# Performance work log

Hardware: AMD Instinct MI355X
Metric: run time of the kernel (lower is better)

## Reference

```python
import jax, jax.numpy as jnp
import numpy as np

D_MODEL = 1024
D_K = 64
D_V = 64
N_HEADS = 16
LN_EPS = 1e-5


def setup_inputs() -> dict:
    key = jax.random.key(0)
    ks = jax.random.split(key, 9)
    B, S = 2, 2048
    scale = 0.02
    return {
        "input_Q": jax.random.normal(ks[0], (B, S, D_MODEL), dtype=jnp.float32),
        "input_K": jax.random.normal(ks[1], (B, S, D_MODEL), dtype=jnp.float32),
        "input_V": jax.random.normal(ks[2], (B, S, D_MODEL), dtype=jnp.float32),
        "W_Q": jax.random.normal(ks[3], (D_MODEL, N_HEADS * D_K), dtype=jnp.float32) * scale,
        "W_K": jax.random.normal(ks[4], (D_MODEL, N_HEADS * D_K), dtype=jnp.float32) * scale,
        "W_V": jax.random.normal(ks[5], (D_MODEL, N_HEADS * D_V), dtype=jnp.float32) * scale,
        "W_O": jax.random.normal(ks[6], (N_HEADS * D_V, D_MODEL), dtype=jnp.float32) * scale,
        "ln_gamma": jnp.ones((D_MODEL,), dtype=jnp.float32),
        "ln_beta": jnp.zeros((D_MODEL,), dtype=jnp.float32),
    }


def reference(input_Q, input_K, input_V, W_Q, W_K, W_V, W_O, ln_gamma, ln_beta):
    B, Lq, _ = input_Q.shape
    Lk = input_K.shape[1]
    # projections -> [B, H, L, d]
    Q = (input_Q @ W_Q).reshape(B, Lq, N_HEADS, D_K).transpose(0, 2, 1, 3)
    K = (input_K @ W_K).reshape(B, Lk, N_HEADS, D_K).transpose(0, 2, 1, 3)
    V = (input_V @ W_V).reshape(B, Lk, N_HEADS, D_V).transpose(0, 2, 1, 3)
    # scores: [B, H, Lq, Lk]
    scores = jnp.einsum("bhqd,bhkd->bhqk", Q, K) / jnp.sqrt(jnp.float32(D_K))
    # NOTE: source uses nn.Softmax(dim=1) -> softmax over the HEADS axis (faithful quirk)
    attn = jax.nn.softmax(scores, axis=1)
    context = jnp.einsum("bhqk,bhkv->bhqv", attn, V)
    context = context.transpose(0, 2, 1, 3).reshape(B, Lq, N_HEADS * D_V)
    output = context @ W_O
    # residual + LayerNorm over last dim
    x = output + input_Q
    mu = jnp.mean(x, axis=-1, keepdims=True)
    var = jnp.mean(jnp.square(x - mu), axis=-1, keepdims=True)
    return (x - mu) / jnp.sqrt(var + LN_EPS) * ln_gamma + ln_beta
```

## Files before the change

### kernel.cpp

```cpp
#include <hip/hip_runtime.h>
#include <cstdint>
#include <cstddef>

#define DM 1024
#define HEADS 16
#define DHEAD 64
#define SEQ 2048
#define BATCH 2

typedef __bf16 bf16x8 __attribute__((ext_vector_type(8)));
typedef float  f32x4  __attribute__((ext_vector_type(4)));
typedef unsigned short u16;
typedef unsigned int u32;
typedef u16 u16x8 __attribute__((ext_vector_type(8)));
typedef u16 u16x4 __attribute__((ext_vector_type(4)));

__device__ __forceinline__ float bf2f(u16 u){
    union { u32 i; float f; } v; v.i = ((u32)u) << 16; return v.f;
}
__device__ __forceinline__ u16 f2bf(float f){
    union { float f; u32 i; } v; v.f = f;
    u32 r = v.i + 0x7FFF + ((v.i >> 16) & 1);
    return (u16)(r >> 16);
}
__device__ __forceinline__ u16 f2bf_rhu(float f){
    union { float f; u32 i; } v; v.f = f;
    return (u16)((v.i + 0x8000u) >> 16);
}
__device__ __forceinline__ void gload16(const u16* g, u16* l){
    __builtin_amdgcn_global_load_lds(
        (const __attribute__((address_space(1))) u32*)g,
        (__attribute__((address_space(3))) u32*)l, 16, 0, 0);
}

__global__ void k_probe(const u16* __restrict__ q, int* __restrict__ hdr){
    if (threadIdx.x == 0 && blockIdx.x == 0){
        int cnt = 0;
        for (int i = 0; i < 256; i += 2){
            int e = (q[i] >> 7) & 0xFF;
            if (e >= 90 && e <= 141) cnt++;
        }
        hdr[0] = (cnt >= 64) ? 1 : 0;
        #pragma unroll
        for (int c = 1; c <= 8; c++) hdr[c] = 0;
    }
}

__global__ __launch_bounds__(256) void k_cvt3(const void* __restrict__ s0,
                                              const void* __restrict__ s1,
                                              const void* __restrict__ s2,
                                              u16* __restrict__ dstbase,
                                              const int* __restrict__ flag, int n){
    int z = blockIdx.y;
    const void* src = (z == 0) ? s0 : ((z == 1) ? s1 : s2);
    u16* dst = dstbase + (size_t)z * n;
    int i = (blockIdx.x * 256 + threadIdx.x) * 8;
    if (i >= n) return;
    if (*flag){
        *(u16x8*)&dst[i] = *(const u16x8*)((const u16*)src + i);
    } else {
        const float* s = (const float*)src + i;
        u16x8 o;
        #pragma unroll
        for (int j = 0; j < 8; j++) o[j] = f2bf(s[j]);
        *(u16x8*)&dst[i] = o;
    }
}

__global__ void k_tcvt4(const void* __restrict__ w0, const void* __restrict__ w1,
                        const void* __restrict__ w2, const void* __restrict__ w3,
                        u16* __restrict__ dstbase,
                        const int* __restrict__ flag, int R, int C){
    __shared__ u16 tile[32][33];
    int z = blockIdx.z;
    const void* src = (z == 0) ? w0 : ((z == 1) ? w1 : ((z == 2) ? w2 : w3));
    u16* dst = dstbase + (size_t)z * R * C;
    bool isbf = (*flag != 0);
    int c0 = blockIdx.x * 32, r0 = blockIdx.y * 32;
    int tx = threadIdx.x, ty = threadIdx.y;
    #pragma unroll
    for (int i = 0; i < 32; i += 8){
        size_t idx = (size_t)(r0 + ty + i) * C + c0 + tx;
        tile[ty + i][tx] = isbf ? ((const u16*)src)[idx] : f2bf(((const float*)src)[idx]);
    }
    __syncthreads();
    #pragma unroll
    for (int i = 0; i < 32; i += 8)
        dst[(size_t)(c0 + ty + i) * R + r0 + tx] = tile[tx][ty + i];
}

__global__ void k_transpose(const u16* __restrict__ src, u16* __restrict__ dst,
                            int R, int C){
    __shared__ u16 tile[32][33];
    size_t boff = (size_t)blockIdx.z * R * C;
    src += boff; dst += boff;
    int c0 = blockIdx.x * 32, r0 = blockIdx.y * 32;
    int tx = threadIdx.x, ty = threadIdx.y;
    #pragma unroll
    for (int i = 0; i < 32; i += 8)
        tile[ty + i][tx] = src[(size_t)(r0 + ty + i) * C + c0 + tx];
    __syncthreads();
    #pragma unroll
    for (int i = 0; i < 32; i += 8)
        dst[(size_t)(c0 + ty + i) * R + r0 + tx] = tile[tx][ty + i];
}

__global__ __launch_bounds__(256, 2) void k_gemm3z(const u16* __restrict__ A0,
                                                   const u16* __restrict__ Bt0,
                                                   u16* __restrict__ C0,
                                                   size_t strA, size_t strB, size_t strC,
                                                   int M, int N, int K){
    __shared__ u16 lsA[128 * 32];
    __shared__ u16 lsB[128 * 32];
    int z = blockIdx.z;
    const u16* A  = A0  + strA * z;
    const u16* Bt = Bt0 + strB * z;
    u16* C = C0 + strC * z;
    int m0 = blockIdx.y * 128, n0 = blockIdx.x * 128;
    int t = threadIdx.x, lane = t & 63, w = t >> 6;
    int l15 = lane & 15, quad = lane >> 4;
    int wm = (w & 1) * 64, wn = (w >> 1) * 64;
    int r0 = 32 * w + (lane >> 2);
    int r1 = r0 + 16;
    int c0s = (lane & 3) ^ (r0 & 3);
    int c1s = (lane & 3) ^ (r1 & 3);
    u16* dA0 = &lsA[(32 * w) * 32];
    u16* dA1 = &lsA[(32 * w + 16) * 32];
    u16* dB0 = &lsB[(32 * w) * 32];
    u16* dB1 = &lsB[(32 * w + 16) * 32];
    f32x4 acc[4][4] = {};
    for (int k0 = 0; k0 < K; k0 += 32){
        __syncthreads();
        gload16(&A [(size_t)(m0 + r0) * K + k0 + c0s * 8], dA0);
        gload16(&A [(size_t)(m0 + r1) * K + k0 + c1s * 8], dA1);
        gload16(&Bt[(size_t)(n0 + r0) * K + k0 + c0s * 8], dB0);
        gload16(&Bt[(size_t)(n0 + r1) * K + k0 + c1s * 8], dB1);
        __syncthreads();
        bf16x8 af[4], bfr[4];
        #pragma unroll
        for (int i = 0; i < 4; i++){
            int row = wm + i * 16 + l15;
            af[i] = *(const bf16x8*)&lsA[row * 32 + ((quad ^ (row & 3)) * 8)];
        }
        #pragma unroll
        for (int j = 0; j < 4; j++){
            int row = wn + j * 16 + l15;
            bfr[j] = *(const bf16x8*)&lsB[row * 32 + ((quad ^ (row & 3)) * 8)];
        }
        #pragma unroll
        for (int i = 0; i < 4; i++)
            #pragma unroll
            for (int j = 0; j < 4; j++)
                acc[i][j] = __builtin_amdgcn_mfma_f32_16x16x32_bf16(af[i], bfr[j], acc[i][j], 0, 0, 0);
    }
    #pragma unroll
    for (int i = 0; i < 4; i++)
        #pragma unroll
        for (int j = 0; j < 4; j++)
            #pragma unroll
            for (int r = 0; r < 4; r++){
                int m = m0 + wm + i * 16 + quad * 4 + r;
                int n = n0 + wn + j * 16 + l15;
                C[(size_t)m * N + n] = f2bf(acc[i][j][r]);
            }
}

__global__ __launch_bounds__(1024, 4) void k_attn5(const u16* __restrict__ Qp,
                                                   const u16* __restrict__ Kp,
                                                   const u16* __restrict__ Vt,
                                                   u16* __restrict__ c0,
                                                   u16* __restrict__ c1,
                                                   u16* __restrict__ c2,
                                                   u16* __restrict__ c3,
                                                   int* __restrict__ cnt,
                                                   int ncomboM1, int iters){
    __shared__ u16 ebuf[2][16][64][36];
    __shared__ int s_combo, s_slot;
    int t = threadIdx.x;
    if (t == 0){
        int xcc;
        asm volatile("s_getreg_b32 %0, hwreg(HW_REG_XCC_ID)" : "=s"(xcc));
        int start = xcc & ncomboM1;
        int combo = -1, slot = -1;
        for (int a = 0; a <= ncomboM1 && combo < 0; a++){
            int c = (start + a) & ncomboM1;
            int s = atomicAdd(&cnt[c], 1);
            if (s < 32){ combo = c; slot = s; }
        }
        s_combo = combo; s_slot = slot;
    }
    __syncthreads();
    int combo = s_combo;
    if (combo < 0) return;
    int b = combo & 1, chunk = combo >> 1;
    int q0 = s_slot * 64;
    int h = t >> 6, lane = t & 63, l15 = lane & 15, quad = lane >> 4;
    u16* outp = (chunk == 0) ? c0 : ((chunk == 1) ? c1 : ((chunk == 2) ? c2 : c3));
    const float cexp = 0.125f * 1.44269504f;
    int kbeg = chunk * (iters << 5);

    bf16x8 qf[4][2];
    #pragma unroll
    for (int sub = 0; sub < 4; sub++)
        #pragma unroll
        for (int ch = 0; ch < 2; ch++)
            qf[sub][ch] = *(const bf16x8*)&Qp[((size_t)(b * SEQ + q0 + sub * 16 + l15)) * DM
                                             + h * DHEAD + ch * 32 + quad * 8];

    f32x4 oacc[4][4] = {};
    int sq = t >> 4, sku = (t & 15) * 2;

    auto score_phase = [&](int it){
        int k0 = kbeg + (it << 5), bf = it & 1;
        #pragma unroll
        for (int kt = 0; kt < 2; kt++){
            const u16* kb = Kp + ((size_t)(b * SEQ + k0 + kt * 16 + l15)) * DM + h * DHEAD + quad * 8;
            bf16x8 kf0 = *(const bf16x8*)(kb);
            bf16x8 kf1 = *(const bf16x8*)(kb + 32);
            #pragma unroll
            for (int sub = 0; sub < 4; sub++){
                f32x4 sc = {};
                sc = __builtin_amdgcn_mfma_f32_16x16x32_bf16(qf[sub][0], kf0, sc, 0, 0, 0);
                sc = __builtin_amdgcn_mfma_f32_16x16x32_bf16(qf[sub][1], kf1, sc, 0, 0, 0);
                #pragma unroll
                for (int r = 0; r < 4; r++)
                    ebuf[bf][h][sub * 16 + quad * 4 + r][kt * 16 + l15] =
                        f2bf_rhu(exp2f(sc[r] * cexp));
            }
        }
    };

    score_phase(0);
    for (int it = 0; it < iters; it++){
        int bf = it & 1;
        __syncthreads();
        if (it + 1 < iters) score_phase(it + 1);
        {
            u32 ev[16];
            float s0 = 0.f, s1 = 0.f;
            #pragma unroll
            for (int hh = 0; hh < 16; hh++){
                u32 u = *(const u32*)&ebuf[bf][hh][sq][sku];
                ev[hh] = u;
                union { u32 i; float f; } lo, hi;
                lo.i = u << 16; hi.i = u & 0xFFFF0000u;
                s0 += lo.f; s1 += hi.f;
            }
            float r0 = __builtin_amdgcn_rcpf(s0);
            float r1 = __builtin_amdgcn_rcpf(s1);
            #pragma unroll
            for (int hh = 0; hh < 16; hh++){
                union { u32 i; float f; } lo, hi, p0, p1;
                lo.i = ev[hh] << 16; hi.i = ev[hh] & 0xFFFF0000u;
                p0.f = lo.f * r0; p1.f = hi.f * r1;
                *(u32*)&ebuf[bf][hh][sq][sku] =
                    ((p0.i + 0x8000u) >> 16) | ((p1.i + 0x8000u) & 0xFFFF0000u);
            }
        }
        __syncthreads();
        int k0 = kbeg + (it << 5);
        bf16x8 pa[4];
        #pragma unroll
        for (int sub = 0; sub < 4; sub++){
            const u16* pp = &ebuf[bf][h][sub * 16 + l15][quad * 8];
            union { bf16x8 v; u16x4 q[2]; } pu;
            pu.q[0] = *(const u16x4*)pp;
            pu.q[1] = *(const u16x4*)(pp + 4);
            pa[sub] = pu.v;
        }
        #pragma unroll
        for (int vt = 0; vt < 4; vt++){
            bf16x8 vf = *(const bf16x8*)&Vt[((size_t)b * DM + h * DHEAD + vt * 16 + l15) * SEQ
                                            + k0 + quad * 8];
            #pragma unroll
            for (int sub = 0; sub < 4; sub++)
                oacc[sub][vt] = __builtin_amdgcn_mfma_f32_16x16x32_bf16(pa[sub], vf, oacc[sub][vt], 0, 0, 0);
        }
    }
    #pragma unroll
    for (int sub = 0; sub < 4; sub++)
        #pragma unroll
        for (int vt = 0; vt < 4; vt++)
            #pragma unroll
            for (int r = 0; r < 4; r++){
                int q = q0 + sub * 16 + quad * 4 + r;
                int n = h * DHEAD + vt * 16 + l15;
                outp[((size_t)b * SEQ + q) * DM + n] = f2bf(oacc[sub][vt][r]);
            }
}

__global__ __launch_bounds__(256) void k_reduce(const u16* __restrict__ a,
                                                const u16* __restrict__ b,
                                                const u16* __restrict__ c,
                                                const u16* __restrict__ d,
                                                u16* __restrict__ dst, int n, int nch){
    int i = (blockIdx.x * 256 + threadIdx.x) * 8;
    if (i >= n) return;
    u16x8 x = *(const u16x8*)&a[i];
    u16x8 y = *(const u16x8*)&b[i];
    u16x8 o;
    if (nch == 4){
        u16x8 zc = *(const u16x8*)&c[i];
        u16x8 zd = *(const u16x8*)&d[i];
        #pragma unroll
        for (int j = 0; j < 8; j++)
            o[j] = f2bf((bf2f(x[j]) + bf2f(y[j])) + (bf2f(zc[j]) + bf2f(zd[j])));
    } else {
        #pragma unroll
        for (int j = 0; j < 8; j++) o[j] = f2bf(bf2f(x[j]) + bf2f(y[j]));
    }
    *(u16x8*)&dst[i] = o;
}

__global__ __launch_bounds__(256) void k_ln(const u16* __restrict__ O,
                                            const void* __restrict__ Qin,
                                            const void* __restrict__ gamma,
                                            const void* __restrict__ beta,
                                            void* __restrict__ out,
                                            const int* __restrict__ flag){
    __shared__ float red[4][2];
    bool isbf = (*flag != 0);
    int row = blockIdx.x;
    int t = threadIdx.x;
    const u16* op = O + (size_t)row * DM;
    float xv[4];
    float s1 = 0.f, s2 = 0.f;
    #pragma unroll
    for (int i = 0; i < 4; i++){
        int idx = i * 256 + t;
        float q = isbf ? bf2f(((const u16*)Qin)[(size_t)row * DM + idx])
                       : ((const float*)Qin)[(size_t)row * DM + idx];
        float x = bf2f(op[idx]) + q;
        xv[i] = x; s1 += x; s2 += x * x;
    }
    #pragma unroll
    for (int off = 32; off; off >>= 1){
        s1 += __shfl_down(s1, off);
        s2 += __shfl_down(s2, off);
    }
    int w = t >> 6, lane = t & 63;
    if (lane == 0){ red[w][0] = s1; red[w][1] = s2; }
    __syncthreads();
    float S1 = red[0][0] + red[1][0] + red[2][0] + red[3][0];
    float S2 = red[0][1] + red[1][1] + red[2][1] + red[3][1];
    float mu  = S1 * (1.0f / DM);
    float var = S2 * (1.0f / DM) - mu * mu;
    float rstd = rsqrtf(var + 1e-5f);
    #pragma unroll
    for (int i = 0; i < 4; i++){
        int idx = i * 256 + t;
        float g = isbf ? bf2f(((const u16*)gamma)[idx]) : ((const float*)gamma)[idx];
        float bb= isbf ? bf2f(((const u16*)beta )[idx]) : ((const float*)beta )[idx];
        float y = (xv[i] - mu) * rstd * g + bb;
        if (isbf) ((u16*)out)[(size_t)row * DM + idx] = f2bf(y);
        else      ((float*)out)[(size_t)row * DM + idx] = y;
    }
}

extern "C" void kernel_launch(void* const* d_in, const int* in_sizes, int n_in,
                              void* d_out, int out_size, void* d_ws, size_t ws_size,
                              hipStream_t stream){
    (void)in_sizes; (void)n_in; (void)out_size;
    const void* inQ = d_in[0];
    const void* inK = d_in[1];
    const void* inV = d_in[2];
    const void* wQ  = d_in[3];
    const void* wK  = d_in[4];
    const void* wV  = d_in[5];
    const void* wO  = d_in[6];
    const void* gma = d_in[7];
    const void* bta = d_in[8];

    int* hdr  = (int*)d_ws;
    int* flag = hdr;
    int* cnt  = hdr + 1;
    u16* base = (u16*)d_ws + 64;

    const size_t MB1 = 1024u * 1024u;
    const size_t M4  = 4u * MB1;
    u16* Qi  = base + 0;
    u16* Ki  = base + 1 * M4;
    u16* Vi  = base + 2 * M4;
    u16* WtQ = base + 3 * M4;
    u16* WtO = WtQ + 3 * MB1;
    u16* Qp  = base + 4 * M4;
    u16* Kp  = base + 5 * M4;
    u16* Vp  = base + 6 * M4;
    u16* ext = base + 7 * M4;
    u16* Vt    = Ki;
    u16* ctxp0 = Qi;
    u16* ctxp1 = Vp;
    u16* ctxp2 = Vi;

    size_t need4 = 128 + 8 * M4 * sizeof(u16);
    int nch = (ws_size >= need4) ? 4 : 2;
    u16* ctxp3 = (nch == 4) ? ext : ctxp2;
    int ncomboM1 = 2 * nch - 1;
    int iters   = (nch == 4) ? 16 : 32;
    int ablocks = 32 * 2 * nch;

    k_probe<<<1, 64, 0, stream>>>((const u16*)inQ, hdr);

    const int nIn = BATCH * SEQ * DM;
    k_cvt3<<<dim3(nIn / 2048, 3), 256, 0, stream>>>(inQ, inK, inV, base, flag, nIn);

    k_tcvt4<<<dim3(32, 32, 4), dim3(32, 8), 0, stream>>>(wQ, wK, wV, wO, WtQ, flag, 1024, 1024);

    k_gemm3z<<<dim3(8, 32, 3), 256, 0, stream>>>(Qi, WtQ, Qp, M4, MB1, M4, 4096, 1024, 1024);

    k_transpose<<<dim3(32, 64, 2), dim3(32, 8), 0, stream>>>(Vp, Vt, 2048, 1024);

    k_attn5<<<ablocks, 1024, 0, stream>>>(Qp, Kp, Vt, ctxp0, ctxp1, ctxp2, ctxp3,
                                          cnt, ncomboM1, iters);

    k_reduce<<<nIn / 2048, 256, 0, stream>>>(ctxp0, ctxp1, ctxp2, ctxp3, ctxp0, nIn, nch);

    k_gemm3z<<<dim3(8, 32, 1), 256, 0, stream>>>(ctxp0, WtO, Qp, 0, 0, 0, 4096, 1024, 1024);

    k_ln<<<4096, 256, 0, stream>>>(Qp, inQ, gma, bta, d_out, flag);
}
```

Measured before the change: 342.9 us.

## Deepen GEMM K-tile, narrow output GEMM tile, reorder attention score prefetch

The GEMM kernel is templated on N-tile width and moves from a K-step of 32 to 64 with an 8-way XOR swizzle, which halves the barrier count per K. The output projection uses a narrower 64-column tile so it launches twice as many blocks. In attention, the next-iteration score phase now runs after the PV MFMAs instead of before the softmax normalisation, exp2f is replaced by raw v_exp_f32 inline asm, and bf16 packing uses v_perm. The probe kernel also zeroes more header slots. The larger LDS tiles may reduce occupancy, and the inline asm can constrain the compiler's scheduling.

```diff
diff --git a/kernel.cpp b/kernel.cpp
--- a/kernel.cpp
+++ b/kernel.cpp
@@ -27,6 +27,11 @@
     union { float f; u32 i; } v; v.f = f;
     return (u16)((v.i + 0x8000u) >> 16);
 }
+__device__ __forceinline__ float fexp2(float x){
+    float r;
+    asm volatile("v_exp_f32 %0, %1\n\ts_nop 1" : "=v"(r) : "v"(x));
+    return r;
+}
 __device__ __forceinline__ void gload16(const u16* g, u16* l){
     __builtin_amdgcn_global_load_lds(
         (const __attribute__((address_space(1))) u32*)g,
@@ -42,7 +47,7 @@
         }
         hdr[0] = (cnt >= 64) ? 1 : 0;
         #pragma unroll
-        for (int c = 1; c <= 8; c++) hdr[c] = 0;
+        for (int c = 1; c <= 24; c++) hdr[c] = 0;
     }
 }
 
@@ -105,63 +110,74 @@
         dst[(size_t)(c0 + ty + i) * R + r0 + tx] = tile[tx][ty + i];
 }
 
-__global__ __launch_bounds__(256, 2) void k_gemm3z(const u16* __restrict__ A0,
-                                                   const u16* __restrict__ Bt0,
-                                                   u16* __restrict__ C0,
-                                                   size_t strA, size_t strB, size_t strC,
-                                                   int M, int N, int K){
-    __shared__ u16 lsA[128 * 32];
-    __shared__ u16 lsB[128 * 32];
+template<int NJ>
+__global__ __launch_bounds__(256, 2) void k_gemmT(const u16* __restrict__ A0,
+                                                  const u16* __restrict__ Bt0,
+                                                  u16* __restrict__ C0,
+                                                  size_t strA, size_t strB, size_t strC,
+                                                  int M, int N, int K){
+    constexpr int BN = NJ * 32;
+    __shared__ u16 lsA[128 * 64];
+    __shared__ u16 lsB[BN * 64];
     int z = blockIdx.z;
     const u16* A  = A0  + strA * z;
     const u16* Bt = Bt0 + strB * z;
     u16* C = C0 + strC * z;
-    int m0 = blockIdx.y * 128, n0 = blockIdx.x * 128;
+    int m0 = blockIdx.y * 128, n0 = blockIdx.x * BN;
     int t = threadIdx.x, lane = t & 63, w = t >> 6;
     int l15 = lane & 15, quad = lane >> 4;
-    int wm = (w & 1) * 64, wn = (w >> 1) * 64;
-    int r0 = 32 * w + (lane >> 2);
-    int r1 = r0 + 16;
-    int c0s = (lane & 3) ^ (r0 & 3);
-    int c1s = (lane & 3) ^ (r1 & 3);
-    u16* dA0 = &lsA[(32 * w) * 32];
-    u16* dA1 = &lsA[(32 * w + 16) * 32];
-    u16* dB0 = &lsB[(32 * w) * 32];
-    u16* dB1 = &lsB[(32 * w + 16) * 32];
-    f32x4 acc[4][4] = {};
-    for (int k0 = 0; k0 < K; k0 += 32){
+    int wm = (w & 1) * 64, wn = (w >> 1) * (NJ * 16);
+    f32x4 acc[4][NJ] = {};
+    for (int k0 = 0; k0 < K; k0 += 64){
         __syncthreads();
-        gload16(&A [(size_t)(m0 + r0) * K + k0 + c0s * 8], dA0);
-        gload16(&A [(size_t)(m0 + r1) * K + k0 + c1s * 8], dA1);
-        gload16(&Bt[(size_t)(n0 + r0) * K + k0 + c0s * 8], dB0);
-        gload16(&Bt[(size_t)(n0 + r1) * K + k0 + c1s * 8], dB1);
+        #pragma unroll
+        for (int j = 0; j < 4; j++){
+            int ub = j * 256 + w * 64;
+            int u  = ub + lane;
+            int r  = u >> 3, cg = (u & 7) ^ (r & 7);
+            gload16(&A[(size_t)(m0 + r) * K + k0 + cg * 8], &lsA[ub * 8]);
+        }
+        #pragma unroll
+        for (int j = 0; j < NJ; j++){
+            int ub = j * 256 + w * 64;
+            int u  = ub + lane;
+            int r  = u >> 3, cg = (u & 7) ^ (r & 7);
+            gload16(&Bt[(size_t)(n0 + r) * K + k0 + cg * 8], &lsB[ub * 8]);
+        }
         __syncthreads();
-        bf16x8 af[4], bfr[4];
+        bf16x8 af[4][2], bfr[NJ][2];
         #pragma unroll
         for (int i = 0; i < 4; i++){
             int row = wm + i * 16 + l15;
-            af[i] = *(const bf16x8*)&lsA[row * 32 + ((quad ^ (row & 3)) * 8)];
-        }
-        #pragma unroll
-        for (int j = 0; j < 4; j++){
-            int row = wn + j * 16 + l15;
-            bfr[j] = *(const bf16x8*)&lsB[row * 32 + ((quad ^ (row & 3)) * 8)];
+            #pragma unroll
+            for (int kk = 0; kk < 2; kk++)
+                af[i][kk] = *(const bf16x8*)&lsA[row * 64 + (((kk * 4 + quad) ^ (row & 7)) * 8)];
+        }
+        #pragma unroll
+        for (int jj = 0; jj < NJ; jj++){
+            int row = wn + jj * 16 + l15;
+            #pragma unroll
+            for (int kk = 0; kk < 2; kk++)
+                bfr[jj][kk] = *(const bf16x8*)&lsB[row * 64 + (((kk * 4 + quad) ^ (row & 7)) * 8)];
         }
         #pragma unroll
         for (int i = 0; i < 4; i++)
             #pragma unroll
-            for (int j = 0; j < 4; j++)
-                acc[i][j] = __builtin_amdgcn_mfma_f32_16x16x32_bf16(af[i], bfr[j], acc[i][j], 0, 0, 0);
+            for (int jj = 0; jj < NJ; jj++)
+                #pragma unroll
+                for (int kk = 0; kk < 2; kk++)
+                    acc[i][jj] = __builtin_amdgcn_mfma_f32_16x16x32_bf16(af[i][kk], bfr[jj][kk],
+                                                                         acc[i][jj], 0, 0, 0);
     }
     #pragma unroll
     for (int i = 0; i < 4; i++)
         #pragma unroll
-        for (int j = 0; j < 4; j++)
+        for (int jj = 0; jj < NJ; jj++)
             #pragma unroll
             for (int r = 0; r < 4; r++){
                 int m = m0 + wm + i * 16 + quad * 4 + r;
-                int n = n0 + wn + j * 16 + l15;
-                C[(size_t)m * N + n] = f2bf(acc[i][j][r]);
+                int n = n0 + wn + jj * 16 + l15;
+                C[(size_t)m * N + n] = f2bf(acc[i][jj][r]);
             }
 }
 
@@ -225,7 +241,7 @@
                 #pragma unroll
                 for (int r = 0; r < 4; r++)
                     ebuf[bf][h][sub * 16 + quad * 4 + r][kt * 16 + l15] =
-                        f2bf_rhu(exp2f(sc[r] * cexp));
+                        f2bf_rhu(fexp2(sc[r] * cexp));
             }
         }
     };
@@ -234,7 +250,6 @@
     for (int it = 0; it < iters; it++){
         int bf = it & 1;
         __syncthreads();
-        if (it + 1 < iters) score_phase(it + 1);
         {
             u32 ev[16];
             float s0 = 0.f, s1 = 0.f;
@@ -254,7 +269,7 @@
                 lo.i = ev[hh] << 16; hi.i = ev[hh] & 0xFFFF0000u;
                 p0.f = lo.f * r0; p1.f = hi.f * r1;
                 *(u32*)&ebuf[bf][hh][sq][sku] =
-                    ((p0.i + 0x8000u) >> 16) | ((p1.i + 0x8000u) & 0xFFFF0000u);
+                    __builtin_amdgcn_perm(p1.i + 0x8000u, p0.i + 0x8000u, 0x07060302u);
             }
         }
         __syncthreads();
@@ -276,6 +291,7 @@
             for (int sub = 0; sub < 4; sub++)
                 oacc[sub][vt] = __builtin_amdgcn_mfma_f32_16x16x32_bf16(pa[sub], vf, oacc[sub][vt], 0, 0, 0);
         }
+        if (it + 1 < iters) score_phase(it + 1);
     }
     #pragma unroll
     for (int sub = 0; sub < 4; sub++)
@@ -406,7 +422,7 @@
 
     k_tcvt4<<<dim3(32, 32, 4), dim3(32, 8), 0, stream>>>(wQ, wK, wV, wO, WtQ, flag, 1024, 1024);
 
-    k_gemm3z<<<dim3(8, 32, 3), 256, 0, stream>>>(Qi, WtQ, Qp, M4, MB1, M4, 4096, 1024, 1024);
+    k_gemmT<4><<<dim3(8, 32, 3), 256, 0, stream>>>(Qi, WtQ, Qp, M4, MB1, M4, 4096, 1024, 1024);
 
     k_transpose<<<dim3(32, 64, 2), dim3(32, 8), 0, stream>>>(Vp, Vt, 2048, 1024);
 
@@ -415,7 +431,7 @@
 
     k_reduce<<<nIn / 2048, 256, 0, stream>>>(ctxp0, ctxp1, ctxp2, ctxp3, ctxp0, nIn, nch);
 
-    k_gemm3z<<<dim3(8, 32, 1), 256, 0, stream>>>(ctxp0, WtO, Qp, 0, 0, 0, 4096, 1024, 1024);
+    k_gemmT<2><<<dim3(16, 32, 1), 256, 0, stream>>>(ctxp0, WtO, Qp, 0, 0, 0, 4096, 1024, 1024);
 
     k_ln<<<4096, 256, 0, stream>>>(Qp, inQ, gma, bta, d_out, flag);
 }
```

Measured after the change: 319.8 us. 6.7% less time.
